# Performance work log

Hardware: AMD Instinct MI355X
Metric: run time of the kernel (lower is better)

The kernel has to match this reference:

```python
import jax, jax.numpy as jnp
import numpy as np

N_HITS = 16384
N_EDGES = 262144
N_GROUPS = 512
N_EVENTS = 64
IN_CH = 25
HID = 128
HEADS = 4
DH = HID // HEADS
LAYERS = 3
EDGE_DIM = 5
FFN = 4 * HID
EPS = 1e-5


def setup_inputs() -> dict:
    key = jax.random.key(0)
    ks = jax.random.split(key, 16)
    def nrm(k, shape, s=0.05):
        return jax.random.normal(k, shape, dtype=jnp.float32) * s
    z = lambda *s: jnp.zeros(s, jnp.float32)
    return {
        "x": jax.random.normal(ks[0], (N_HITS, IN_CH), dtype=jnp.float32),
        "edge_index": jax.random.randint(ks[1], (2, N_EDGES), 0, N_HITS, dtype=jnp.int32),
        "edge_attr": jax.random.normal(ks[2], (N_EDGES, EDGE_DIM), dtype=jnp.float32),
        "group_indices": jax.random.randint(ks[3], (N_HITS,), 0, N_GROUPS, dtype=jnp.int32),
        "batch_indices_per_group": jnp.sort(jax.random.randint(ks[4], (N_GROUPS,), 0, N_EVENTS, dtype=jnp.int32)),
        "embed_W": nrm(ks[5], (IN_CH, HID)),
        "embed_b": z(HID),
        "blk_Wqkv": nrm(ks[6], (LAYERS, HID, 3 * HID)),
        "blk_bqkv": z(LAYERS, 3 * HID),
        "blk_We": nrm(ks[7], (LAYERS, EDGE_DIM, HID)),
        "blk_be": z(LAYERS, HID),
        "blk_Wo": nrm(ks[8], (LAYERS, HID, HID)),
        "blk_bo": z(LAYERS, HID),
        "ln1_g": jnp.ones((LAYERS, HID), jnp.float32),
        "ln1_b": z(LAYERS, HID),
        "ffn_W1": nrm(ks[9], (LAYERS, HID, FFN)),
        "ffn_b1": z(LAYERS, FFN),
        "ffn_W2": nrm(ks[10], (LAYERS, FFN, HID)),
        "ffn_b2": z(LAYERS, HID),
        "ln2_g": jnp.ones((LAYERS, HID), jnp.float32),
        "ln2_b": z(LAYERS, HID),
        "aff_W1": nrm(ks[11], (4 * HID, HID)),
        "aff_b1": z(HID),
        "aff_W2": nrm(ks[12], (HID, 1)),
        "aff_b2": z(1),
    }


def _layer_norm(v, g, b):
    mu = jnp.mean(v, axis=-1, keepdims=True)
    var = jnp.mean((v - mu) ** 2, axis=-1, keepdims=True)
    return (v - mu) * jax.lax.rsqrt(var + EPS) * g + b


def reference(x, edge_index, edge_attr, group_indices, batch_indices_per_group,
              embed_W, embed_b, blk_Wqkv, blk_bqkv, blk_We, blk_be, blk_Wo, blk_bo,
              ln1_g, ln1_b, ffn_W1, ffn_b1, ffn_W2, ffn_b2, ln2_g, ln2_b,
              aff_W1, aff_b1, aff_W2, aff_b2):
    n = x.shape[0]
    G = batch_indices_per_group.shape[0]
    src, dst = edge_index[0], edge_index[1]
    scale = 1.0 / np.sqrt(DH).astype(np.float32)

    h = x @ embed_W + embed_b  # [N, HID]
    for l in range(LAYERS):
        # edge-conditioned multi-head attention over the graph edges
        qkv = h @ blk_Wqkv[l] + blk_bqkv[l]
        q, k, v = jnp.split(qkv, 3, axis=-1)
        e = edge_attr @ blk_We[l] + blk_be[l]          # [E, HID]
        qe = q[dst].reshape(-1, HEADS, DH)              # [E, h, d]
        ke = (k[src] + e).reshape(-1, HEADS, DH)
        ve = (v[src] + e).reshape(-1, HEADS, DH)
        logits = jnp.einsum("ehd,ehd->eh", qe, ke) * scale
        m = jax.ops.segment_max(logits, dst, num_segments=n)
        m = jnp.where(jnp.isfinite(m), m, 0.0)          # nodes with no in-edges
        p = jnp.exp(logits - m[dst])
        s = jax.ops.segment_sum(p, dst, num_segments=n)
        attn = jax.ops.segment_sum(p[:, :, None] * ve, dst, num_segments=n)
        attn = (attn / jnp.maximum(s, 1e-9)[:, :, None]).reshape(n, HID)
        h = _layer_norm(h + attn @ blk_Wo[l] + blk_bo[l], ln1_g[l], ln1_b[l])
        f = jax.nn.relu(h @ ffn_W1[l] + ffn_b1[l]) @ ffn_W2[l] + ffn_b2[l]
        h = _layer_norm(h + f, ln2_g[l], ln2_b[l])

    # group pooling (multi-scatter)
    raw_view = x[:, 3].astype(jnp.int32)  # truncation, matches torch .long()
    cnt_all = jax.ops.segment_sum(jnp.ones((n,), jnp.float32), group_indices, num_segments=G)
    g_max = jax.ops.segment_max(h, group_indices, num_segments=G)
    g_max = jnp.where(cnt_all[:, None] > 0, g_max, 0.0)  # torch_scatter fills empty with 0

    def pool_view(view_id):
        w = (raw_view == view_id).astype(jnp.float32)
        cnt = jax.ops.segment_sum(w, group_indices, num_segments=G)
        summ = jax.ops.segment_sum(h * w[:, None], group_indices, num_segments=G)
        pooled = summ / jnp.maximum(cnt, 1.0)[:, None]
        has = (cnt > 0).astype(jnp.float32)[:, None]
        return pooled, has

    pool_x, has_x = pool_view(0)
    pool_y, has_y = pool_view(1)
    sum_feat = pool_x * has_x + pool_y * has_y
    valid = jnp.maximum(has_x + has_y, 1.0)
    ge = jnp.concatenate([sum_feat / valid, g_max], axis=1)  # [G, 2*HID]

    # pairwise affinity MLP: Linear(4H->H) split so the [G,G,4H] concat is never built
    W1a, W1b = aff_W1[: 2 * HID], aff_W1[2 * HID:]
    pre = (ge @ W1a)[:, None, :] + (ge @ W1b)[None, :, :] + aff_b1  # [G, G, HID]
    scores = (jax.nn.relu(pre) @ aff_W2 + aff_b2)[..., 0]           # [G, G]
    scores = 0.5 * (scores + scores.T)
    event_mask = batch_indices_per_group[:, None] == batch_indices_per_group[None, :]
    return jax.nn.sigmoid(scores) * event_mask.astype(scores.dtype)
```

## Files before the change

### kernel.cpp

```cpp
#include <hip/hip_runtime.h>
#include <hip/hip_bf16.h>

#define NHITS   16384
#define NEDGES  262144
#define NGROUPS 512
#define HID     128
#define LAYERS  3
#define FFND    512
#define MAXDEG  64
#define GCAP    96

typedef __attribute__((ext_vector_type(8))) short bf16x8;
typedef __attribute__((ext_vector_type(8))) unsigned short ushort8;
typedef __attribute__((ext_vector_type(4))) float floatx4;

__device__ __forceinline__ float bf2f(ushort u) {
    return __uint_as_float(((unsigned)u) << 16);
}
__device__ __forceinline__ ushort f2bf(float f) {
    unsigned u = __float_as_uint(f);
    unsigned r = (u + 0x7FFFu + ((u >> 16) & 1u)) >> 16;
    return (ushort)r;
}

__device__ __forceinline__ void gl2lds16(const ushort* gp, ushort* lp) {
    __builtin_amdgcn_global_load_lds(
        (const __attribute__((address_space(1))) unsigned int*)(gp),
        (__attribute__((address_space(3))) unsigned int*)(lp), 16, 0, 0);
}


struct TD { const float* src; ushort* dst; int K; int N; };
struct TDs { TD d[14]; };

__global__ __launch_bounds__(256) void transpose_all(TDs tds, int* __restrict__ zbuf,
                                                     int ztotal) {
    __shared__ float lds[32][33];
    if (blockIdx.y == 0) {
        for (int gz = blockIdx.x * 256 + threadIdx.x; gz < ztotal; gz += 64 * 256)
            zbuf[gz] = 0;
    }
    TD d = tds.d[blockIdx.y];
    int tX = d.N >> 5;
    int tiles = (d.K >> 5) * tX;
    if ((int)blockIdx.x >= tiles) return;
    int tk = blockIdx.x / tX, tn = blockIdx.x % tX;
    int k0 = tk * 32, n0 = tn * 32;
    int r = threadIdx.x >> 5, c = threadIdx.x & 31;
#pragma unroll
    for (int i = 0; i < 4; ++i)
        lds[r + i * 8][c] = d.src[(size_t)(k0 + r + i * 8) * d.N + n0 + c];
    __syncthreads();
#pragma unroll
    for (int i = 0; i < 4; ++i) {
        int n = n0 + r + i * 8;
        d.dst[(size_t)n * d.K + k0 + c] = f2bf(lds[c][r + i * 8]);
    }
}


__global__ __launch_bounds__(256) void scatter_embed(
        const int* __restrict__ src, const int* __restrict__ dst,
        const float* __restrict__ ea, const int* __restrict__ gidx,
        int* __restrict__ cnt, int* __restrict__ cnt2,
        int* __restrict__ ps, float* __restrict__ pea, int* __restrict__ hlist,
        const float* __restrict__ x, const float* __restrict__ embW,
        const float* __restrict__ embB, float* __restrict__ h,
        ushort* __restrict__ hb) {
    const int vb = blockIdx.x, t = threadIdx.x;
    if (vb < 1024) {
        int e = vb * 256 + t;
        int d = dst[e];
        int slot = atomicAdd(&cnt[d], 1);
        if (slot < MAXDEG) {
            size_t pos = (size_t)d * MAXDEG + slot;
            ps[pos] = src[e];
#pragma unroll
            for (int j = 0; j < 5; ++j) pea[pos * 5 + j] = ea[(size_t)e * 5 + j];
        }
        if (e < NHITS) {
            int g = gidx[e];
            int slot2 = atomicAdd(&cnt2[g], 1);
            if (slot2 < GCAP) hlist[g * GCAP + slot2] = e;
        }
    } else {
        __shared__ float xs[2][32];
        int base = (vb - 1024) * 32;
        for (int it = 0; it < 16; ++it) {
            int i0 = base + it * 2;
            __syncthreads();
            if (t < 25) xs[0][t] = x[(size_t)i0 * 25 + t];
            else if (t >= 128 && t < 153) xs[1][t - 128] = x[(size_t)(i0 + 1) * 25 + (t - 128)];
            __syncthreads();
            int node = i0 + (t >> 7), c = t & 127;
            const float* xr = xs[t >> 7];
            float s = embB[c];
#pragma unroll
            for (int k = 0; k < 25; ++k) s += xr[k] * embW[k * HID + c];
            h[(size_t)node * HID + c] = s;
            hb[(size_t)node * HID + c] = f2bf(s);
        }
    }
}


__global__ __launch_bounds__(256) void gemm_mfma_k(const ushort* __restrict__ A,
                                                   const ushort* __restrict__ Bt,
                                                   const float* __restrict__ bias,
                                                   ushort* __restrict__ C,
                                                   int N, int K, int relu) {
    __shared__ ushort As[128 * 32];
    __shared__ ushort Bs[128 * 32];
    const int t = threadIdx.x;
    const int lane = t & 63;
    const int w = t >> 6;
    const int wr = w >> 1, wc = w & 1;
    const int lm = lane & 15, q = lane >> 4;
    const int row0 = blockIdx.y * 128;
    const int col0 = blockIdx.x * 128;
    const int sr = t >> 2, sc = (t & 3) * 8;
    const int sr2 = (t + 256) >> 2, sc2 = ((t + 256) & 3) * 8;

    floatx4 acc[4][4] = {};
    for (int k0 = 0; k0 < K; k0 += 32) {
        gl2lds16(A + (size_t)(row0 + sr) * K + k0 + sc,   &As[t * 8]);
        gl2lds16(A + (size_t)(row0 + sr2) * K + k0 + sc2, &As[t * 8 + 2048]);
        gl2lds16(Bt + (size_t)(col0 + sr) * K + k0 + sc,   &Bs[t * 8]);
        gl2lds16(Bt + (size_t)(col0 + sr2) * K + k0 + sc2, &Bs[t * 8 + 2048]);
        __syncthreads();
        bf16x8 af[4], bf[4];
#pragma unroll
        for (int it = 0; it < 4; ++it)
            af[it] = *(const bf16x8*)&As[(wr * 64 + it * 16 + lm) * 32 + q * 8];
#pragma unroll
        for (int jt = 0; jt < 4; ++jt)
            bf[jt] = *(const bf16x8*)&Bs[(wc * 64 + jt * 16 + lm) * 32 + q * 8];
#pragma unroll
        for (int it = 0; it < 4; ++it)
#pragma unroll
            for (int jt = 0; jt < 4; ++jt)
                acc[it][jt] = __builtin_amdgcn_mfma_f32_16x16x32_bf16(
                    af[it], bf[jt], acc[it][jt], 0, 0, 0);
        __syncthreads();
    }
#pragma unroll
    for (int jt = 0; jt < 4; ++jt) {
        int col = col0 + wc * 64 + jt * 16 + lm;
        float bb = bias ? bias[col] : 0.f;
#pragma unroll
        for (int it = 0; it < 4; ++it)
#pragma unroll
            for (int r = 0; r < 4; ++r) {
                int row = row0 + wr * 64 + it * 16 + q * 4 + r;
                float o = acc[it][jt][r] + bb;
                if (relu) o = fmaxf(o, 0.f);
                C[(size_t)row * N + col] = f2bf(o);
            }
    }
}


__global__ __launch_bounds__(256) void attn_kernel(const ushort* __restrict__ qkv,
                                                   const int* __restrict__ ps,
                                                   const float* __restrict__ pea,
                                                   const int* __restrict__ cnt,
                                                   const float* __restrict__ We,
                                                   const float* __restrict__ be,
                                                   ushort* __restrict__ attnb) {
    __shared__ float WeS[640], beS[128];
    int t = threadIdx.x;
    for (int idx = t; idx < 640; idx += 256) WeS[idx] = We[idx];
    if (t < 128) beS[t] = be[t];
    __syncthreads();
    const int i = blockIdx.x * 4 + (t >> 6);
    const int lane = t & 63;
    const int grp = lane >> 4;
    const int cb = (lane & 15) * 8;
    float qv[8];
    {
        ushort8 qq = *(const ushort8*)(qkv + (size_t)i * 384 + cb);
#pragma unroll
        for (int j = 0; j < 8; ++j) qv[j] = bf2f(qq[j]);
    }
    float pj[6];
#pragma unroll
    for (int k = 0; k < 5; ++k) {
        float s = 0.f;
#pragma unroll
        for (int j = 0; j < 8; ++j) s += qv[j] * WeS[k * 128 + cb + j];
        pj[k] = s;
    }
    {
        float sb = 0.f;
#pragma unroll
        for (int j = 0; j < 8; ++j) sb += qv[j] * beS[cb + j];
        pj[5] = sb;
    }
#pragma unroll
    for (int k = 0; k < 6; ++k) {
        pj[k] += __shfl_xor(pj[k], 1);
        pj[k] += __shfl_xor(pj[k], 2);
    }
    float S = 0.f, T0 = 0.f, T1 = 0.f, T2 = 0.f, T3 = 0.f, T4 = 0.f;
    float acc[8] = {};
    const int endc = min(cnt[i], MAXDEG);
    const size_t pbase = (size_t)i * MAXDEG;
    const float scale = 0.17677669529663687f;

#pragma unroll 4
    for (int p0 = 0; p0 < endc; p0 += 4) {
        int pp = p0 + grp;
        bool act = pp < endc;
        int slot = act ? pp : (endc - 1);
        int s = ps[pbase + slot];
        const float* eap = pea + (pbase + slot) * 5;
        float a0 = eap[0], a1 = eap[1], a2 = eap[2], a3 = eap[3], a4 = eap[4];
        const ushort* srow = qkv + (size_t)s * 384;
        ushort8 kk = *(const ushort8*)(srow + 128 + cb);
        ushort8 vv = *(const ushort8*)(srow + 256 + cb);
        float part = 0.f;
#pragma unroll
        for (int j = 0; j < 8; ++j) part += qv[j] * bf2f(kk[j]);
        part += __shfl_xor(part, 1);
        part += __shfl_xor(part, 2);
        float logit = (part + pj[5] + a0 * pj[0] + a1 * pj[1] + a2 * pj[2]
                       + a3 * pj[3] + a4 * pj[4]) * scale;
        float pe = act ? __expf(logit) : 0.f;
        S += pe;
        T0 += pe * a0; T1 += pe * a1; T2 += pe * a2; T3 += pe * a3; T4 += pe * a4;
#pragma unroll
        for (int j = 0; j < 8; ++j) acc[j] += pe * bf2f(vv[j]);
    }
#pragma unroll
    for (int j = 0; j < 8; ++j) {
        acc[j] += __shfl_xor(acc[j], 16);
        acc[j] += __shfl_xor(acc[j], 32);
    }
    S += __shfl_xor(S, 16);   S += __shfl_xor(S, 32);
    T0 += __shfl_xor(T0, 16); T0 += __shfl_xor(T0, 32);
    T1 += __shfl_xor(T1, 16); T1 += __shfl_xor(T1, 32);
    T2 += __shfl_xor(T2, 16); T2 += __shfl_xor(T2, 32);
    T3 += __shfl_xor(T3, 16); T3 += __shfl_xor(T3, 32);
    T4 += __shfl_xor(T4, 16); T4 += __shfl_xor(T4, 32);
    if (grp == 0) {
        float inv = 1.f / fmaxf(S, 1e-9f);
        ushort8 o;
#pragma unroll
        for (int j = 0; j < 8; ++j) {
            float wadd = WeS[cb + j] * T0 + WeS[128 + cb + j] * T1
                       + WeS[256 + cb + j] * T2 + WeS[384 + cb + j] * T3
                       + WeS[512 + cb + j] * T4 + beS[cb + j] * S;
            o[j] = f2bf((acc[j] + wadd) * inv);
        }
        *(ushort8*)(attnb + (size_t)i * HID + cb) = o;
    }
}


__global__ __launch_bounds__(256) void gemm_ln_k(const ushort* __restrict__ A,
                                                 const ushort* __restrict__ Bt,
                                                 const float* __restrict__ bias,
                                                 const float* __restrict__ g,
                                                 const float* __restrict__ b,
                                                 float* __restrict__ h,
                                                 ushort* __restrict__ hb,
                                                 int K) {
    __shared__ ushort As[32 * 32];
    __shared__ ushort Bs[128 * 32];
    __shared__ float redS[64], redQ[64];
    const int t = threadIdx.x;
    const int lane = t & 63;
    const int w = t >> 6;
    const int wr = w >> 1, wc = w & 1;
    const int lm = lane & 15, q = lane >> 4;
    const int row0 = blockIdx.x * 32;
    const int sr = t >> 2, sc = (t & 3) * 8;
    const int sr2 = (t + 256) >> 2, sc2 = ((t + 256) & 3) * 8;

    floatx4 acc[4] = {};
    for (int k0 = 0; k0 < K; k0 += 32) {
        if (t < 128)
            gl2lds16(A + (size_t)(row0 + sr) * K + k0 + sc, &As[t * 8]);
        gl2lds16(Bt + (size_t)sr * K + k0 + sc,   &Bs[t * 8]);
        gl2lds16(Bt + (size_t)sr2 * K + k0 + sc2, &Bs[t * 8 + 2048]);
        __syncthreads();
        bf16x8 af = *(const bf16x8*)&As[(wr * 16 + lm) * 32 + q * 8];
        bf16x8 bf[4];
#pragma unroll
        for (int jt = 0; jt < 4; ++jt)
            bf[jt] = *(const bf16x8*)&Bs[(wc * 64 + jt * 16 + lm) * 32 + q * 8];
#pragma unroll
        for (int jt = 0; jt < 4; ++jt)
            acc[jt] = __builtin_amdgcn_mfma_f32_16x16x32_bf16(af, bf[jt], acc[jt], 0, 0, 0);
        __syncthreads();
    }
    float psum[4] = {}, psq[4] = {};
#pragma unroll
    for (int jt = 0; jt < 4; ++jt) {
        int col = wc * 64 + jt * 16 + lm;
        float bb = bias[col];
#pragma unroll
        for (int r = 0; r < 4; ++r) {
            int row = row0 + wr * 16 + q * 4 + r;
            float v = acc[jt][r] + bb + h[(size_t)row * HID + col];
            acc[jt][r] = v;
            psum[r] += v;
            psq[r] += v * v;
        }
    }
#pragma unroll
    for (int r = 0; r < 4; ++r) {
        float s = psum[r], ss = psq[r];
#pragma unroll
        for (int k = 1; k < 16; k <<= 1) {
            s += __shfl_xor(s, k, 16);
            ss += __shfl_xor(ss, k, 16);
        }
        psum[r] = s; psq[r] = ss;
    }
    if (lm == 0)
#pragma unroll
        for (int r = 0; r < 4; ++r) {
            int rl = wr * 16 + q * 4 + r;
            redS[rl * 2 + wc] = psum[r];
            redQ[rl * 2 + wc] = psq[r];
        }
    __syncthreads();
#pragma unroll
    for (int r = 0; r < 4; ++r) {
        int rl = wr * 16 + q * 4 + r;
        float tot = redS[rl * 2] + redS[rl * 2 + 1];
        float totq = redQ[rl * 2] + redQ[rl * 2 + 1];
        float mu = tot * (1.f / HID);
        float var = totq * (1.f / HID) - mu * mu;
        float rstd = rsqrtf(var + 1e-5f);
        int row = row0 + rl;
#pragma unroll
        for (int jt = 0; jt < 4; ++jt) {
            int col = wc * 64 + jt * 16 + lm;
            float o = (acc[jt][r] - mu) * rstd * g[col] + b[col];
            h[(size_t)row * HID + col] = o;
            hb[(size_t)row * HID + col] = f2bf(o);
        }
    }
}


__global__ __launch_bounds__(256) void ffn_k(const ushort* __restrict__ hbuf,
                                             const ushort* __restrict__ W1t,
                                             const float* __restrict__ b1v,
                                             const ushort* __restrict__ W2t,
                                             const float* __restrict__ b2v,
                                             const float* __restrict__ g,
                                             const float* __restrict__ b,
                                             float* __restrict__ h,
                                             ushort* __restrict__ hb) {
    __shared__ ushort As[32 * 136];
    __shared__ ushort Bs[128 * 32];
    __shared__ ushort mid[32 * 520];
    __shared__ float redS[64], redQ[64];
    const int t = threadIdx.x;
    const int lane = t & 63;
    const int w = t >> 6;
    const int wr = w >> 1, wc = w & 1;
    const int lm = lane & 15, q = lane >> 4;
    const int row0 = blockIdx.x * 32;
    const int sr = t >> 2, sc = (t & 3) * 8;
    const int sr2 = (t + 256) >> 2, sc2 = ((t + 256) & 3) * 8;

    for (int i = t; i < 32 * 16; i += 256) {
        int row = i >> 4, c8 = (i & 15) * 8;
        *(ushort8*)&As[row * 136 + c8] =
            *(const ushort8*)(hbuf + (size_t)(row0 + row) * HID + c8);
    }
    __syncthreads();

    for (int nc = 0; nc < 4; ++nc) {
        floatx4 acc1[4] = {};
        for (int k0 = 0; k0 < 128; k0 += 32) {
            gl2lds16(W1t + (size_t)(nc * 128 + sr) * HID + k0 + sc,   &Bs[t * 8]);
            gl2lds16(W1t + (size_t)(nc * 128 + sr2) * HID + k0 + sc2, &Bs[t * 8 + 2048]);
            __syncthreads();
            bf16x8 af = *(const bf16x8*)&As[(wr * 16 + lm) * 136 + k0 + q * 8];
#pragma unroll
            for (int jt = 0; jt < 4; ++jt) {
                bf16x8 bf = *(const bf16x8*)&Bs[(wc * 64 + jt * 16 + lm) * 32 + q * 8];
                acc1[jt] = __builtin_amdgcn_mfma_f32_16x16x32_bf16(af, bf, acc1[jt], 0, 0, 0);
            }
            __syncthreads();
        }
#pragma unroll
        for (int jt = 0; jt < 4; ++jt) {
            int col = wc * 64 + jt * 16 + lm;
            float bb = b1v[nc * 128 + col];
#pragma unroll
            for (int r = 0; r < 4; ++r) {
                int row = wr * 16 + q * 4 + r;
                mid[row * 520 + nc * 128 + col] = f2bf(fmaxf(acc1[jt][r] + bb, 0.f));
            }
        }
    }
    __syncthreads();

    floatx4 acc2[4] = {};
    for (int k0 = 0; k0 < 512; k0 += 32) {
        gl2lds16(W2t + (size_t)sr * FFND + k0 + sc,   &Bs[t * 8]);
        gl2lds16(W2t + (size_t)sr2 * FFND + k0 + sc2, &Bs[t * 8 + 2048]);
        __syncthreads();
        bf16x8 af = *(const bf16x8*)&mid[(wr * 16 + lm) * 520 + k0 + q * 8];
#pragma unroll
        for (int jt = 0; jt < 4; ++jt) {
            bf16x8 bf = *(const bf16x8*)&Bs[(wc * 64 + jt * 16 + lm) * 32 + q * 8];
            acc2[jt] = __builtin_amdgcn_mfma_f32_16x16x32_bf16(af, bf, acc2[jt], 0, 0, 0);
        }
        __syncthreads();
    }

    float psum[4] = {}, psq[4] = {};
#pragma unroll
    for (int jt = 0; jt < 4; ++jt) {
        int col = wc * 64 + jt * 16 + lm;
        float bb = b2v[col];
#pragma unroll
        for (int r = 0; r < 4; ++r) {
            int row = row0 + wr * 16 + q * 4 + r;
            float v = acc2[jt][r] + bb + h[(size_t)row * HID + col];
            acc2[jt][r] = v;
            psum[r] += v;
            psq[r] += v * v;
        }
    }
#pragma unroll
    for (int r = 0; r < 4; ++r) {
        float s = psum[r], ss = psq[r];
#pragma unroll
        for (int k = 1; k < 16; k <<= 1) {
            s += __shfl_xor(s, k, 16);
            ss += __shfl_xor(ss, k, 16);
        }
        psum[r] = s; psq[r] = ss;
    }
    if (lm == 0)
#pragma unroll
        for (int r = 0; r < 4; ++r) {
            int rl = wr * 16 + q * 4 + r;
            redS[rl * 2 + wc] = psum[r];
            redQ[rl * 2 + wc] = psq[r];
        }
    __syncthreads();
#pragma unroll
    for (int r = 0; r < 4; ++r) {
        int rl = wr * 16 + q * 4 + r;
        float tot = redS[rl * 2] + redS[rl * 2 + 1];
        float totq = redQ[rl * 2] + redQ[rl * 2 + 1];
        float mu = tot * (1.f / HID);
        float var = totq * (1.f / HID) - mu * mu;
        float rstd = rsqrtf(var + 1e-5f);
        int row = row0 + rl;
#pragma unroll
        for (int jt = 0; jt < 4; ++jt) {
            int col = wc * 64 + jt * 16 + lm;
            float o = (acc2[jt][r] - mu) * rstd * g[col] + b[col];
            h[(size_t)row * HID + col] = o;
            hb[(size_t)row * HID + col] = f2bf(o);
        }
    }
}


__global__ __launch_bounds__(128) void pool_group(const float* __restrict__ h,
                                                  const float* __restrict__ x,
                                                  const int* __restrict__ hlist,
                                                  const int* __restrict__ cnt2,
                                                  ushort* __restrict__ geb) {
    int g = blockIdx.x, c = threadIdx.x;
    int n = min(cnt2[g], GCAP);
    float mx = -INFINITY, sx = 0.f, sy = 0.f, cx = 0.f, cy = 0.f;
    for (int p = 0; p < n; ++p) {
        int i = hlist[g * GCAP + p];
        float hv = h[(size_t)i * HID + c];
        mx = fmaxf(mx, hv);
        int view = (int)x[(size_t)i * 25 + 3];
        if (view == 0) { sx += hv; cx += 1.f; }
        else if (view == 1) { sy += hv; cy += 1.f; }
    }
    float gm = (n > 0) ? mx : 0.f;
    float px = sx / fmaxf(cx, 1.f), py = sy / fmaxf(cy, 1.f);
    float hx = cx > 0.f ? 1.f : 0.f, hy = cy > 0.f ? 1.f : 0.f;
    float sf = px * hx + py * hy;
    float valid = fmaxf(hx + hy, 1.f);
    geb[g * 256 + c] = f2bf(sf / valid);
    geb[g * 256 + 128 + c] = f2bf(gm);
}


__global__ __launch_bounds__(256) void score_final(const ushort* __restrict__ Cab,
                                                   const float* __restrict__ W2,
                                                   const float* __restrict__ b1v,
                                                   const float* __restrict__ b2,
                                                   const int* __restrict__ ev,
                                                   float* __restrict__ out) {
    int bi = blockIdx.y, bj = blockIdx.x;
    if (bj < bi) return;
    __shared__ float Ai[16][129], Bi[16][129], Aj[16][129], Bj[16][129];
    __shared__ float w2s[128], b1s[128];
    int t = threadIdx.y * 16 + threadIdx.x;
    int i0 = bi * 16, j0 = bj * 16;
    for (int idx = t; idx < 2048; idx += 256) {
        int r = idx >> 7, k = idx & 127;
        Ai[r][k] = bf2f(Cab[(size_t)(i0 + r) * 256 + k]);
        Bi[r][k] = bf2f(Cab[(size_t)(i0 + r) * 256 + 128 + k]);
        Aj[r][k] = bf2f(Cab[(size_t)(j0 + r) * 256 + k]);
        Bj[r][k] = bf2f(Cab[(size_t)(j0 + r) * 256 + 128 + k]);
    }
    if (t < 128) { w2s[t] = W2[t]; b1s[t] = b1v[t]; }
    __syncthreads();
    int tx = threadIdx.x, ty = threadIdx.y;
    float sij = 0.f, sji = 0.f;
#pragma unroll 4
    for (int k = 0; k < 128; ++k) {
        float pb = b1s[k], wk = w2s[k];
        sij += fmaxf(Ai[ty][k] + Bj[tx][k] + pb, 0.f) * wk;
        sji += fmaxf(Aj[tx][k] + Bi[ty][k] + pb, 0.f) * wk;
    }
    float z = 0.5f * (sij + sji) + b2[0];
    float sg = 1.f / (1.f + __expf(-z));
    int gi = i0 + ty, gj = j0 + tx;
    float res = (ev[gi] == ev[gj]) ? sg : 0.f;
    out[(size_t)gi * NGROUPS + gj] = res;
    out[(size_t)gj * NGROUPS + gi] = res;
}


static inline char* align256(char* p) {
    return (char*)(((uintptr_t)p + 255) & ~(uintptr_t)255);
}

extern "C" void kernel_launch(void* const* d_in, const int* in_sizes, int n_in,
                              void* d_out, int out_size, void* d_ws, size_t ws_size,
                              hipStream_t stream) {
    const float* x    = (const float*)d_in[0];
    const int* eidx   = (const int*)d_in[1];
    const float* ea   = (const float*)d_in[2];
    const int* gidx   = (const int*)d_in[3];
    const int* ev     = (const int*)d_in[4];
    const float* embW = (const float*)d_in[5];
    const float* embB = (const float*)d_in[6];
    const float* Wqkv = (const float*)d_in[7];
    const float* bqkv = (const float*)d_in[8];
    const float* We   = (const float*)d_in[9];
    const float* be   = (const float*)d_in[10];
    const float* Wo   = (const float*)d_in[11];
    const float* bo   = (const float*)d_in[12];
    const float* ln1g = (const float*)d_in[13];
    const float* ln1b = (const float*)d_in[14];
    const float* W1   = (const float*)d_in[15];
    const float* b1   = (const float*)d_in[16];
    const float* W2   = (const float*)d_in[17];
    const float* b2   = (const float*)d_in[18];
    const float* ln2g = (const float*)d_in[19];
    const float* ln2b = (const float*)d_in[20];
    const float* affW1 = (const float*)d_in[21];
    const float* affb1 = (const float*)d_in[22];
    const float* affW2 = (const float*)d_in[23];
    const float* affb2 = (const float*)d_in[24];

    const int* src = eidx;
    const int* dst = eidx + NEDGES;

    char* p = (char*)d_ws;
    float* h    = (float*)p;            p += (size_t)NHITS * HID * 4;
    float* pea  = (float*)p;            p += (size_t)NHITS * MAXDEG * 5 * 4;
    int* cnt    = (int*)p;              p += NHITS * 4;
    int* cnt2   = (int*)p;              p += NGROUPS * 4;
    int* ps     = (int*)p;              p += (size_t)NHITS * MAXDEG * 4;
    int* hlist  = (int*)p;              p += NGROUPS * GCAP * 4;
    p = align256(p);
    ushort* hb    = (ushort*)p;         p += (size_t)NHITS * HID * 2;
    ushort* qkvb  = (ushort*)p;         p += (size_t)NHITS * 384 * 2;
    ushort* attnb = (ushort*)p;         p += (size_t)NHITS * HID * 2;
    ushort* geb   = (ushort*)p;         p += (size_t)NGROUPS * 256 * 2;
    ushort* Cab   = (ushort*)p;         p += (size_t)NGROUPS * 256 * 2;
    p = align256(p);
    ushort* Wqkvt = (ushort*)p;         p += (size_t)LAYERS * 384 * HID * 2;
    ushort* Wot   = (ushort*)p;         p += (size_t)LAYERS * HID * HID * 2;
    ushort* W1t   = (ushort*)p;         p += (size_t)LAYERS * FFND * HID * 2;
    ushort* W2t   = (ushort*)p;         p += (size_t)LAYERS * HID * FFND * 2;
    ushort* W1abt = (ushort*)p;         p += (size_t)256 * 256 * 2;

    TDs tds;
    for (int l = 0; l < LAYERS; ++l) {
        tds.d[l * 4 + 0] = { Wqkv + (size_t)l * HID * 384, Wqkvt + (size_t)l * 384 * HID, HID, 384 };
        tds.d[l * 4 + 1] = { Wo + (size_t)l * HID * HID,   Wot + (size_t)l * HID * HID,   HID, HID };
        tds.d[l * 4 + 2] = { W1 + (size_t)l * HID * FFND,  W1t + (size_t)l * FFND * HID,  HID, FFND };
        tds.d[l * 4 + 3] = { W2 + (size_t)l * FFND * HID,  W2t + (size_t)l * HID * FFND,  FFND, HID };
    }
    tds.d[12] = { affW1,             W1abt,             256, HID };
    tds.d[13] = { affW1 + 256 * HID, W1abt + 128 * 256, 256, HID };
    transpose_all<<<dim3(64, 14), 256, 0, stream>>>(tds, cnt, NHITS + NGROUPS);

    scatter_embed<<<1536, 256, 0, stream>>>(src, dst, ea, gidx, cnt, cnt2,
                                            ps, pea, hlist, x, embW, embB, h, hb);

    for (int l = 0; l < LAYERS; ++l) {
        gemm_mfma_k<<<dim3(3, NHITS / 128), 256, 0, stream>>>(
            hb, Wqkvt + (size_t)l * 384 * HID, bqkv + l * 384, qkvb, 384, HID, 0);
        attn_kernel<<<NHITS / 4, 256, 0, stream>>>(
            qkvb, ps, pea, cnt, We + (size_t)l * 5 * HID, be + l * HID, attnb);
        gemm_ln_k<<<NHITS / 32, 256, 0, stream>>>(
            attnb, Wot + (size_t)l * HID * HID, bo + l * HID,
            ln1g + l * HID, ln1b + l * HID, h, hb, HID);
        ffn_k<<<NHITS / 32, 256, 0, stream>>>(
            hb, W1t + (size_t)l * FFND * HID, b1 + l * FFND,
            W2t + (size_t)l * HID * FFND, b2 + l * HID,
            ln2g + l * HID, ln2b + l * HID, h, hb);
    }

    pool_group<<<NGROUPS, 128, 0, stream>>>(h, x, hlist, cnt2, geb);
    gemm_mfma_k<<<dim3(2, NGROUPS / 128), 256, 0, stream>>>(
        geb, W1abt, nullptr, Cab, 256, 256, 0);
    score_final<<<dim3(NGROUPS / 16, NGROUPS / 16), dim3(16, 16), 0, stream>>>(
        Cab, affW2, affb1, affb2, ev, (float*)d_out);
}
```

Measured before the change: 373.2 us.

## Fuse output projection and LayerNorm into FFN kernel; split Q from KV buffer

Merges the attention output projection, residual add and first LayerNorm into the FFN kernel, so the intermediate h/hb round-trip and one launch per layer go away. The post-LN1 activations stay in registers (o1) and shared memory for the FFN residual. The QKV GEMM now writes Q and a packed K|V buffer separately, so gathered neighbor rows in attention are 512 bytes instead of strided within 768-byte rows, which improves locality. The cost is higher register and shared-memory pressure in the fused kernel.

```diff
diff --git a/kernel.cpp b/kernel.cpp
--- a/kernel.cpp
+++ b/kernel.cpp
@@ -160,7 +160,66 @@
 }
 
 
-__global__ __launch_bounds__(256) void attn_kernel(const ushort* __restrict__ qkv,
+__global__ __launch_bounds__(256) void gemm_qkv_k(const ushort* __restrict__ A,
+                                                  const ushort* __restrict__ Bt,
+                                                  const float* __restrict__ bias,
+                                                  ushort* __restrict__ qb,
+                                                  ushort* __restrict__ kvb,
+                                                  int K) {
+    __shared__ ushort As[128 * 32];
+    __shared__ ushort Bs[128 * 32];
+    const int t = threadIdx.x;
+    const int lane = t & 63;
+    const int w = t >> 6;
+    const int wr = w >> 1, wc = w & 1;
+    const int lm = lane & 15, q = lane >> 4;
+    const int row0 = blockIdx.y * 128;
+    const int col0 = blockIdx.x * 128;
+    const int sr = t >> 2, sc = (t & 3) * 8;
+    const int sr2 = (t + 256) >> 2, sc2 = ((t + 256) & 3) * 8;
+
+    floatx4 acc[4][4] = {};
+    for (int k0 = 0; k0 < K; k0 += 32) {
+        gl2lds16(A + (size_t)(row0 + sr) * K + k0 + sc,   &As[t * 8]);
+        gl2lds16(A + (size_t)(row0 + sr2) * K + k0 + sc2, &As[t * 8 + 2048]);
+        gl2lds16(Bt + (size_t)(col0 + sr) * K + k0 + sc,   &Bs[t * 8]);
+        gl2lds16(Bt + (size_t)(col0 + sr2) * K + k0 + sc2, &Bs[t * 8 + 2048]);
+        __syncthreads();
+        bf16x8 af[4], bf[4];
+#pragma unroll
+        for (int it = 0; it < 4; ++it)
+            af[it] = *(const bf16x8*)&As[(wr * 64 + it * 16 + lm) * 32 + q * 8];
+#pragma unroll
+        for (int jt = 0; jt < 4; ++jt)
+            bf[jt] = *(const bf16x8*)&Bs[(wc * 64 + jt * 16 + lm) * 32 + q * 8];
+#pragma unroll
+        for (int it = 0; it < 4; ++it)
+#pragma unroll
+            for (int jt = 0; jt < 4; ++jt)
+                acc[it][jt] = __builtin_amdgcn_mfma_f32_16x16x32_bf16(
+                    af[it], bf[jt], acc[it][jt], 0, 0, 0);
+        __syncthreads();
+    }
+#pragma unroll
+    for (int jt = 0; jt < 4; ++jt) {
+        int col = col0 + wc * 64 + jt * 16 + lm;
+        float bb = bias[col];
+#pragma unroll
+        for (int it = 0; it < 4; ++it)
+#pragma unroll
+            for (int r = 0; r < 4; ++r) {
+                int row = row0 + wr * 64 + it * 16 + q * 4 + r;
+                float o = acc[it][jt][r] + bb;
+                ushort ob = f2bf(o);
+                if (col < 128) qb[(size_t)row * 128 + col] = ob;
+                else           kvb[(size_t)row * 256 + (col - 128)] = ob;
+            }
+    }
+}
+
+
+__global__ __launch_bounds__(256) void attn_kernel(const ushort* __restrict__ qb,
+                                                   const ushort* __restrict__ kvb,
                                                    const int* __restrict__ ps,
                                                    const float* __restrict__ pea,
                                                    const int* __restrict__ cnt,
@@ -178,7 +237,7 @@
     const int cb = (lane & 15) * 8;
     float qv[8];
     {
-        ushort8 qq = *(const ushort8*)(qkv + (size_t)i * 384 + cb);
+        ushort8 qq = *(const ushort8*)(qb + (size_t)i * 128 + cb);
 #pragma unroll
         for (int j = 0; j < 8; ++j) qv[j] = bf2f(qq[j]);
     }
@@ -215,9 +274,9 @@
         int s = ps[pbase + slot];
         const float* eap = pea + (pbase + slot) * 5;
         float a0 = eap[0], a1 = eap[1], a2 = eap[2], a3 = eap[3], a4 = eap[4];
-        const ushort* srow = qkv + (size_t)s * 384;
-        ushort8 kk = *(const ushort8*)(srow + 128 + cb);
-        ushort8 vv = *(const ushort8*)(srow + 256 + cb);
+        const ushort* srow = kvb + (size_t)s * 256;
+        ushort8 kk = *(const ushort8*)(srow + cb);
+        ushort8 vv = *(const ushort8*)(srow + 128 + cb);
         float part = 0.f;
 #pragma unroll
         for (int j = 0; j < 8; ++j) part += qv[j] * bf2f(kk[j]);
@@ -257,104 +316,14 @@
 }
 
 
-__global__ __launch_bounds__(256) void gemm_ln_k(const ushort* __restrict__ A,
-                                                 const ushort* __restrict__ Bt,
-                                                 const float* __restrict__ bias,
-                                                 const float* __restrict__ g,
-                                                 const float* __restrict__ b,
-                                                 float* __restrict__ h,
-                                                 ushort* __restrict__ hb,
-                                                 int K) {
-    __shared__ ushort As[32 * 32];
-    __shared__ ushort Bs[128 * 32];
-    __shared__ float redS[64], redQ[64];
-    const int t = threadIdx.x;
-    const int lane = t & 63;
-    const int w = t >> 6;
-    const int wr = w >> 1, wc = w & 1;
-    const int lm = lane & 15, q = lane >> 4;
-    const int row0 = blockIdx.x * 32;
-    const int sr = t >> 2, sc = (t & 3) * 8;
-    const int sr2 = (t + 256) >> 2, sc2 = ((t + 256) & 3) * 8;
-
-    floatx4 acc[4] = {};
-    for (int k0 = 0; k0 < K; k0 += 32) {
-        if (t < 128)
-            gl2lds16(A + (size_t)(row0 + sr) * K + k0 + sc, &As[t * 8]);
-        gl2lds16(Bt + (size_t)sr * K + k0 + sc,   &Bs[t * 8]);
-        gl2lds16(Bt + (size_t)sr2 * K + k0 + sc2, &Bs[t * 8 + 2048]);
-        __syncthreads();
-        bf16x8 af = *(const bf16x8*)&As[(wr * 16 + lm) * 32 + q * 8];
-        bf16x8 bf[4];
-#pragma unroll
-        for (int jt = 0; jt < 4; ++jt)
-            bf[jt] = *(const bf16x8*)&Bs[(wc * 64 + jt * 16 + lm) * 32 + q * 8];
-#pragma unroll
-        for (int jt = 0; jt < 4; ++jt)
-            acc[jt] = __builtin_amdgcn_mfma_f32_16x16x32_bf16(af, bf[jt], acc[jt], 0, 0, 0);
-        __syncthreads();
-    }
-    float psum[4] = {}, psq[4] = {};
-#pragma unroll
-    for (int jt = 0; jt < 4; ++jt) {
-        int col = wc * 64 + jt * 16 + lm;
-        float bb = bias[col];
-#pragma unroll
-        for (int r = 0; r < 4; ++r) {
-            int row = row0 + wr * 16 + q * 4 + r;
-            float v = acc[jt][r] + bb + h[(size_t)row * HID + col];
-            acc[jt][r] = v;
-            psum[r] += v;
-            psq[r] += v * v;
-        }
-    }
-#pragma unroll
-    for (int r = 0; r < 4; ++r) {
-        float s = psum[r], ss = psq[r];
-#pragma unroll
-        for (int k = 1; k < 16; k <<= 1) {
-            s += __shfl_xor(s, k, 16);
-            ss += __shfl_xor(ss, k, 16);
-        }
-        psum[r] = s; psq[r] = ss;
-    }
-    if (lm == 0)
-#pragma unroll
-        for (int r = 0; r < 4; ++r) {
-            int rl = wr * 16 + q * 4 + r;
-            redS[rl * 2 + wc] = psum[r];
-            redQ[rl * 2 + wc] = psq[r];
-        }
-    __syncthreads();
-#pragma unroll
-    for (int r = 0; r < 4; ++r) {
-        int rl = wr * 16 + q * 4 + r;
-        float tot = redS[rl * 2] + redS[rl * 2 + 1];
-        float totq = redQ[rl * 2] + redQ[rl * 2 + 1];
-        float mu = tot * (1.f / HID);
-        float var = totq * (1.f / HID) - mu * mu;
-        float rstd = rsqrtf(var + 1e-5f);
-        int row = row0 + rl;
-#pragma unroll
-        for (int jt = 0; jt < 4; ++jt) {
-            int col = wc * 64 + jt * 16 + lm;
-            float o = (acc[jt][r] - mu) * rstd * g[col] + b[col];
-            h[(size_t)row * HID + col] = o;
-            hb[(size_t)row * HID + col] = f2bf(o);
-        }
-    }
-}
-
-
-__global__ __launch_bounds__(256) void ffn_k(const ushort* __restrict__ hbuf,
-                                             const ushort* __restrict__ W1t,
-                                             const float* __restrict__ b1v,
-                                             const ushort* __restrict__ W2t,
-                                             const float* __restrict__ b2v,
-                                             const float* __restrict__ g,
-                                             const float* __restrict__ b,
-                                             float* __restrict__ h,
-                                             ushort* __restrict__ hb) {
+__global__ __launch_bounds__(256) void woffn_k(
+        const ushort* __restrict__ attnb,
+        const ushort* __restrict__ Wot, const float* __restrict__ bo,
+        const float* __restrict__ ln1g, const float* __restrict__ ln1b,
+        const ushort* __restrict__ W1t, const float* __restrict__ b1v,
+        const ushort* __restrict__ W2t, const float* __restrict__ b2v,
+        const float* __restrict__ ln2g, const float* __restrict__ ln2b,
+        float* __restrict__ h, ushort* __restrict__ hb) {
     __shared__ ushort As[32 * 136];
     __shared__ ushort Bs[128 * 32];
     __shared__ ushort mid[32 * 520];
@@ -371,7 +340,73 @@
     for (int i = t; i < 32 * 16; i += 256) {
         int row = i >> 4, c8 = (i & 15) * 8;
         *(ushort8*)&As[row * 136 + c8] =
-            *(const ushort8*)(hbuf + (size_t)(row0 + row) * HID + c8);
+            *(const ushort8*)(attnb + (size_t)(row0 + row) * HID + c8);
+    }
+    __syncthreads();
+
+    floatx4 accW[4] = {};
+    for (int k0 = 0; k0 < 128; k0 += 32) {
+        gl2lds16(Wot + (size_t)sr * HID + k0 + sc,   &Bs[t * 8]);
+        gl2lds16(Wot + (size_t)sr2 * HID + k0 + sc2, &Bs[t * 8 + 2048]);
+        __syncthreads();
+        bf16x8 af = *(const bf16x8*)&As[(wr * 16 + lm) * 136 + k0 + q * 8];
+#pragma unroll
+        for (int jt = 0; jt < 4; ++jt) {
+            bf16x8 bf = *(const bf16x8*)&Bs[(wc * 64 + jt * 16 + lm) * 32 + q * 8];
+            accW[jt] = __builtin_amdgcn_mfma_f32_16x16x32_bf16(af, bf, accW[jt], 0, 0, 0);
+        }
+        __syncthreads();
+    }
+    float o1[4][4];
+    {
+        float psum[4] = {}, psq[4] = {};
+#pragma unroll
+        for (int jt = 0; jt < 4; ++jt) {
+            int col = wc * 64 + jt * 16 + lm;
+            float bb = bo[col];
+#pragma unroll
+            for (int r = 0; r < 4; ++r) {
+                int row = row0 + wr * 16 + q * 4 + r;
+                float v = accW[jt][r] + bb + h[(size_t)row * HID + col];
+                o1[jt][r] = v;
+                psum[r] += v;
+                psq[r] += v * v;
+            }
+        }
+#pragma unroll
+        for (int r = 0; r < 4; ++r) {
+            float s = psum[r], ss = psq[r];
+#pragma unroll
+            for (int k = 1; k < 16; k <<= 1) {
+                s += __shfl_xor(s, k, 16);
+                ss += __shfl_xor(ss, k, 16);
+            }
+            psum[r] = s; psq[r] = ss;
+        }
+        if (lm == 0)
+#pragma unroll
+            for (int r = 0; r < 4; ++r) {
+                int rl = wr * 16 + q * 4 + r;
+                redS[rl * 2 + wc] = psum[r];
+                redQ[rl * 2 + wc] = psq[r];
+            }
+        __syncthreads();
+#pragma unroll
+        for (int r = 0; r < 4; ++r) {
+            int rl = wr * 16 + q * 4 + r;
+            float tot = redS[rl * 2] + redS[rl * 2 + 1];
+            float totq = redQ[rl * 2] + redQ[rl * 2 + 1];
+            float mu = tot * (1.f / HID);
+            float var = totq * (1.f / HID) - mu * mu;
+            float rstd = rsqrtf(var + 1e-5f);
+#pragma unroll
+            for (int jt = 0; jt < 4; ++jt) {
+                int col = wc * 64 + jt * 16 + lm;
+                float o = (o1[jt][r] - mu) * rstd * ln1g[col] + ln1b[col];
+                o1[jt][r] = o;
+                As[(wr * 16 + q * 4 + r) * 136 + col] = f2bf(o);
+            }
+        }
     }
     __syncthreads();
 
@@ -415,7 +450,6 @@
         }
         __syncthreads();
     }
-
     float psum[4] = {}, psq[4] = {};
 #pragma unroll
     for (int jt = 0; jt < 4; ++jt) {
@@ -423,8 +457,7 @@
         float bb = b2v[col];
 #pragma unroll
         for (int r = 0; r < 4; ++r) {
-            int row = row0 + wr * 16 + q * 4 + r;
-            float v = acc2[jt][r] + bb + h[(size_t)row * HID + col];
+            float v = acc2[jt][r] + bb + o1[jt][r];
             acc2[jt][r] = v;
             psum[r] += v;
             psq[r] += v * v;
@@ -460,7 +493,7 @@
 #pragma unroll
         for (int jt = 0; jt < 4; ++jt) {
             int col = wc * 64 + jt * 16 + lm;
-            float o = (acc2[jt][r] - mu) * rstd * g[col] + b[col];
+            float o = (acc2[jt][r] - mu) * rstd * ln2g[col] + ln2b[col];
             h[(size_t)row * HID + col] = o;
             hb[(size_t)row * HID + col] = f2bf(o);
         }
@@ -577,7 +610,8 @@
     int* hlist  = (int*)p;              p += NGROUPS * GCAP * 4;
     p = align256(p);
     ushort* hb    = (ushort*)p;         p += (size_t)NHITS * HID * 2;
-    ushort* qkvb  = (ushort*)p;         p += (size_t)NHITS * 384 * 2;
+    ushort* qb    = (ushort*)p;         p += (size_t)NHITS * 128 * 2;
+    ushort* kvb   = (ushort*)p;         p += (size_t)NHITS * 256 * 2;
     ushort* attnb = (ushort*)p;         p += (size_t)NHITS * HID * 2;
     ushort* geb   = (ushort*)p;         p += (size_t)NGROUPS * 256 * 2;
     ushort* Cab   = (ushort*)p;         p += (size_t)NGROUPS * 256 * 2;
@@ -603,15 +637,14 @@
                                             ps, pea, hlist, x, embW, embB, h, hb);
 
     for (int l = 0; l < LAYERS; ++l) {
-        gemm_mfma_k<<<dim3(3, NHITS / 128), 256, 0, stream>>>(
-            hb, Wqkvt + (size_t)l * 384 * HID, bqkv + l * 384, qkvb, 384, HID, 0);
+        gemm_qkv_k<<<dim3(3, NHITS / 128), 256, 0, stream>>>(
+            hb, Wqkvt + (size_t)l * 384 * HID, bqkv + l * 384, qb, kvb, HID);
         attn_kernel<<<NHITS / 4, 256, 0, stream>>>(
-            qkvb, ps, pea, cnt, We + (size_t)l * 5 * HID, be + l * HID, attnb);
-        gemm_ln_k<<<NHITS / 32, 256, 0, stream>>>(
+            qb, kvb, ps, pea, cnt, We + (size_t)l * 5 * HID, be + l * HID, attnb);
+        woffn_k<<<NHITS / 32, 256, 0, stream>>>(
             attnb, Wot + (size_t)l * HID * HID, bo + l * HID,
-            ln1g + l * HID, ln1b + l * HID, h, hb, HID);
-        ffn_k<<<NHITS / 32, 256, 0, stream>>>(
-            hb, W1t + (size_t)l * FFND * HID, b1 + l * FFND,
+            ln1g + l * HID, ln1b + l * HID,
+            W1t + (size_t)l * FFND * HID, b1 + l * FFND,
             W2t + (size_t)l * HID * FFND, b2 + l * HID,
             ln2g + l * HID, ln2b + l * HID, h, hb);
     }
```

After: 361.2 us. -3.2%, faster.
